# Kernel tuning notes

Hardware: AMD Instinct MI355X
Metric: run time of the kernel (lower is better)

Reference implementation:

```python
import jax, jax.numpy as jnp
import numpy as np

B = 65536
IN = 64
OUT = 256
D = 4
P = D * (D + 1) // 2  # total (w1, W2) pairs across all terms


def setup_inputs() -> dict:
    key = jax.random.key(0)
    ks = jax.random.split(key, 6)
    s = 1.0 / np.sqrt(IN)
    return {
        "x": jax.random.normal(ks[0], (B, IN), dtype=jnp.float32),
        "d0": jax.random.uniform(ks[1], (1, OUT), dtype=jnp.float32, minval=-s, maxval=s),
        "d1t_w": jax.random.uniform(ks[2], (OUT, IN), dtype=jnp.float32, minval=-s, maxval=s),
        "d1_w": jax.random.uniform(ks[3], (D, OUT, IN), dtype=jnp.float32, minval=-s, maxval=s),
        "dn_w1": jax.random.uniform(ks[4], (P, IN), dtype=jnp.float32, minval=-s, maxval=s),
        "dn_w2": jax.random.uniform(ks[5], (P, OUT, IN), dtype=jnp.float32, minval=-s, maxval=s),
    }


def reference(x, d0, d1t_w, d1_w, dn_w1, dn_w2):
    # res = d0 + d1t(x) + sum_i (x @ d1_i.T) * prod_{j<=i} (x @ (W2_ij * w1_ij).T)
    # The factorization (x @ (W2 * w1).T) is exactly equal to the original
    # Linear(in,1)(tmp_dt * (tx * W2)) chain, without the [B,out,in] intermediate.
    res = d0 + x @ d1t_w.T  # [B, OUT]
    p = 0
    for i in range(D):
        tmp = x @ d1_w[i].T  # [B, OUT]
        for _ in range(i + 1):
            M = dn_w2[p] * dn_w1[p][None, :]  # [OUT, IN]
            tmp = tmp * (x @ M.T)             # [B, OUT]
            p += 1
        res = res + tmp
    return res
```

## Files before the change

kernel.cpp:

```cpp
#include <hip/hip_runtime.h>
#include <hip/hip_bf16.h>

#define BATCH 65536
#define INF   64
#define OUTF  256
#define NMAT  15
#define RPB   256
#define LDSW  68

typedef __bf16 bf16x8 __attribute__((ext_vector_type(8)));
typedef float  f32x4  __attribute__((ext_vector_type(4)));

__device__ __forceinline__ unsigned short f2bf(float f) {
    unsigned int u = __float_as_uint(f);
    unsigned int r = (u + 0x7FFFu + ((u >> 16) & 1u)) >> 16;
    return (unsigned short)r;
}

__device__ __forceinline__ void wload(bf16x8& d, const void* p) {
    asm volatile("global_load_dwordx4 %0, %1, off" : "=v"(d) : "v"(p));
}

__global__ void build_weights(const float* __restrict__ d1t_w,
                              const float* __restrict__ d1_w,
                              const float* __restrict__ dn_w1,
                              const float* __restrict__ dn_w2,
                              unsigned short* __restrict__ wcs) {
    const int idx = blockIdx.x * 256 + threadIdx.x;
    if (idx >= NMAT * OUTF * INF / 8) return;
    const signed char kind[NMAT] = {0,1,2,1,2,2,1,2,2,2,1,2,2,2,2};
    const signed char sidx[NMAT] = {0,0,0,1,1,2,2,3,4,5,3,6,7,8,9};
    const int slot = idx >> 11, rem8 = idx & 2047;
    const int o = rem8 >> 3, cc = rem8 & 7;
    const int s = cc >> 2, g = cc & 3;
    const int i0 = cc * 8;
    const int cs = o >> 4, l = o & 15;
    const int k = kind[slot], si = sidx[slot];
    unsigned short o8[8];
#pragma unroll
    for (int j = 0; j < 8; ++j) {
        const int e = o * INF + i0 + j;
        float v;
        if (k == 0)      v = d1t_w[e];
        else if (k == 1) v = d1_w[si * OUTF * INF + e];
        else             v = dn_w2[si * OUTF * INF + e] * dn_w1[si * INF + i0 + j];
        o8[j] = f2bf(v);
    }
    char* dst = (char*)wcs + (((size_t)slot * 16 + cs) * 2 + s) * 1024 + g * 256 + l * 16;
    *(bf16x8*)dst = *(bf16x8*)o8;
}

__global__ __launch_bounds__(512, 4) void taylor_kernel(
    const float* __restrict__ x, const float* __restrict__ d0w,
    const unsigned short* __restrict__ wcs, float* __restrict__ out)
{
    __shared__ char  xsh[32768];
    __shared__ float sbuf[2][2][32 * LDSW];

    const int lane  = threadIdx.x & 63;
    const int wv    = threadIdx.x >> 6;
    const int strip = wv >> 1;
    const int role  = wv & 1;
    const int l15   = lane & 15;
    const int g     = lane >> 4;
    const int cg    = blockIdx.x >> 8;
    const int rc    = blockIdx.x & 255;
    const int cs    = cg * 4 + strip;

    const int MA[8] = {0, 1, 2, 6, 7, 8, 9, 9};
    const int MB[8] = {3, 4, 5, 10, 11, 12, 13, 14};
    bf16x8 b[8][2];
    const char* wb0 = (const char*)wcs + lane * 16;
#pragma unroll
    for (int i = 0; i < 8; ++i) {
        const int m = role ? MB[i] : MA[i];
        if (role == 0 && i == 7) continue;
        const char* wp = wb0 + (((size_t)m * 16 + cs) * 2) * 1024;
        wload(b[i][0], wp);
        wload(b[i][1], wp + 1024);
    }

    const size_t row0 = (size_t)rc * RPB;

    {
        const float* xsrc = x + row0 * INF;
#pragma unroll
        for (int j = 0; j < 4; ++j) {
            const int c = j * 512 + (int)threadIdx.x;
            f32x4 v0 = *(const f32x4*)(xsrc + (size_t)c * 8);
            f32x4 v1 = *(const f32x4*)(xsrc + (size_t)c * 8 + 4);
            bf16x8 fr;
#pragma unroll
            for (int q = 0; q < 4; ++q) { fr[q] = (__bf16)v0[q]; fr[4 + q] = (__bf16)v1[q]; }
            const int row = c >> 3, cc = c & 7;
            const int ss = cc >> 2, gg = cc & 3;
            const int grp = row >> 4, r_ = row & 15;
            const int rx = r_ ^ ((ss * 4 + gg) & 7);
            *(bf16x8*)(xsh + grp * 2048 + ss * 1024 + gg * 256 + rx * 16) = fr;
        }
    }

    asm volatile("s_waitcnt vmcnt(0)" ::: "memory");
    __builtin_amdgcn_sched_barrier(0);
    __syncthreads();

    const f32x4 d0v = *(const f32x4*)(d0w + cs * 16 + g * 4);
    const int x0off = (l15 ^ g) * 16;
    const int x1off = (l15 ^ (4 + g)) * 16;

#pragma unroll
    for (int t = 0; t < 8; ++t) {
        const char* pg0 = xsh + (t * 2) * 2048 + g * 256;
        const char* pg1 = pg0 + 2048;
        bf16x8 u00 = *(const bf16x8*)(pg0 + x0off);
        bf16x8 u01 = *(const bf16x8*)(pg0 + 1024 + x1off);
        bf16x8 u10 = *(const bf16x8*)(pg1 + x0off);
        bf16x8 u11 = *(const bf16x8*)(pg1 + 1024 + x1off);

        f32x4 res0, res1, tmp0, tmp1, y0, y1;
        const f32x4 z = {0.f, 0.f, 0.f, 0.f};
        __builtin_amdgcn_s_setprio(1);
#define Y4(bi, c0)                                                                  \
        y0 = __builtin_amdgcn_mfma_f32_16x16x32_bf16(b[bi][0], u00, c0, 0, 0, 0);   \
        y1 = __builtin_amdgcn_mfma_f32_16x16x32_bf16(b[bi][0], u10, c0, 0, 0, 0);   \
        y0 = __builtin_amdgcn_mfma_f32_16x16x32_bf16(b[bi][1], u01, y0, 0, 0, 0);   \
        y1 = __builtin_amdgcn_mfma_f32_16x16x32_bf16(b[bi][1], u11, y1, 0, 0, 0);
        if (role == 0) {
            Y4(0, d0v) res0 = y0; res1 = y1;
            Y4(1, z)   tmp0 = y0; tmp1 = y1;
            Y4(2, z)   tmp0 *= y0; tmp1 *= y1; res0 += tmp0; res1 += tmp1;
            Y4(3, z)   tmp0 = y0; tmp1 = y1;
            Y4(4, z)   tmp0 *= y0; tmp1 *= y1;
            Y4(5, z)   tmp0 *= y0; tmp1 *= y1;
            Y4(6, z)   tmp0 *= y0; tmp1 *= y1; res0 += tmp0; res1 += tmp1;
        } else {
            Y4(0, z)   tmp0 = y0; tmp1 = y1;
            Y4(1, z)   tmp0 *= y0; tmp1 *= y1;
            Y4(2, z)   tmp0 *= y0; tmp1 *= y1; res0 = tmp0; res1 = tmp1;
            Y4(3, z)   tmp0 = y0; tmp1 = y1;
            Y4(4, z)   tmp0 *= y0; tmp1 *= y1;
            Y4(5, z)   tmp0 *= y0; tmp1 *= y1;
            Y4(6, z)   tmp0 *= y0; tmp1 *= y1;
            Y4(7, z)   tmp0 *= y0; tmp1 *= y1; res0 += tmp0; res1 += tmp1;
        }
#undef Y4
        __builtin_amdgcn_s_setprio(0);

        float* sb = &sbuf[t & 1][role][0];
        const int colw = strip * 16 + g * 4;
        *(f32x4*)&sb[l15 * LDSW + colw]        = res0;
        *(f32x4*)&sb[(16 + l15) * LDSW + colw] = res1;
        asm volatile("s_waitcnt lgkmcnt(0)\n\ts_barrier" ::: "memory");

        const float* pA = &sbuf[t & 1][0][0];
        const float* pB = &sbuf[t & 1][1][0];
        const int rr = threadIdx.x >> 4;
        const int c4 = (threadIdx.x & 15) * 4;
        f32x4 v = *(const f32x4*)&pA[rr * LDSW + c4];
        v = v + *(const f32x4*)&pB[rr * LDSW + c4];
        float* op = out + (row0 + (size_t)t * 32 + rr) * OUTF + cg * 64 + c4;
        __builtin_nontemporal_store(v, (f32x4*)op);
    }
}

extern "C" void kernel_launch(void* const* d_in, const int* in_sizes, int n_in,
                              void* d_out, int out_size, void* d_ws, size_t ws_size,
                              hipStream_t stream) {
    const float* x    = (const float*)d_in[0];
    const float* d0   = (const float*)d_in[1];
    const float* d1t  = (const float*)d_in[2];
    const float* d1w  = (const float*)d_in[3];
    const float* dnw1 = (const float*)d_in[4];
    const float* dnw2 = (const float*)d_in[5];
    unsigned short* wcs = (unsigned short*)d_ws;
    float* out = (float*)d_out;

    build_weights<<<(NMAT * OUTF * INF / 8 + 255) / 256, 256, 0, stream>>>(
        d1t, d1w, dnw1, dnw2, wcs);
    taylor_kernel<<<4 * (BATCH / RPB), 512, 0, stream>>>(x, d0, wcs, out);
}
```

Measured before the change: 41.01 us.

## Split work into three balanced wave roles with narrower column groups

The block shrinks to 6 waves: 2 column strips with 3 roles each, so every wave runs exactly 5 weight matrices instead of 7 or 8 per role. The grid doubles to 8 column groups of 32 output columns, and each block reduces three partial LDS buffers before its store. MFMA chains use two independent accumulator pairs for more instruction-level parallelism, and the weight-load wait moves ahead of x staging. In exchange, each row block of x is loaded and converted to bf16 twice as often, and only 256 of 384 threads do the final store.

```diff
diff --git a/kernel.cpp b/kernel.cpp
--- a/kernel.cpp
+++ b/kernel.cpp
@@ -6,7 +6,7 @@
 #define OUTF  256
 #define NMAT  15
 #define RPB   256
-#define LDSW  68
+#define LDSW  36
 
 typedef __bf16 bf16x8 __attribute__((ext_vector_type(8)));
 typedef float  f32x4  __attribute__((ext_vector_type(4)));
@@ -50,58 +50,60 @@
     *(bf16x8*)dst = *(bf16x8*)o8;
 }
 
-__global__ __launch_bounds__(512, 4) void taylor_kernel(
+__global__ __launch_bounds__(384, 4) void taylor_kernel(
     const float* __restrict__ x, const float* __restrict__ d0w,
     const unsigned short* __restrict__ wcs, float* __restrict__ out)
 {
     __shared__ char  xsh[32768];
-    __shared__ float sbuf[2][2][32 * LDSW];
+    __shared__ float sbuf[2][3][32 * LDSW];
 
     const int lane  = threadIdx.x & 63;
     const int wv    = threadIdx.x >> 6;
-    const int strip = wv >> 1;
-    const int role  = wv & 1;
+    const int strip = (wv >= 3) ? 1 : 0;
+    const int role  = wv - 3 * strip;
     const int l15   = lane & 15;
     const int g     = lane >> 4;
     const int cg    = blockIdx.x >> 8;
     const int rc    = blockIdx.x & 255;
-    const int cs    = cg * 4 + strip;
-
-    const int MA[8] = {0, 1, 2, 6, 7, 8, 9, 9};
-    const int MB[8] = {3, 4, 5, 10, 11, 12, 13, 14};
-    bf16x8 b[8][2];
+    const int cs    = cg * 2 + strip;
+
+    const int M0a[5] = {0, 6, 7, 8, 9};
+    const int M1a[5] = {1, 2, 3, 4, 5};
+    const int M2a[5] = {10, 11, 12, 13, 14};
+    bf16x8 b[5][2];
     const char* wb0 = (const char*)wcs + lane * 16;
 #pragma unroll
-    for (int i = 0; i < 8; ++i) {
-        const int m = role ? MB[i] : MA[i];
-        if (role == 0 && i == 7) continue;
+    for (int i = 0; i < 5; ++i) {
+        const int m = (role == 0) ? M0a[i] : (role == 1) ? M1a[i] : M2a[i];
         const char* wp = wb0 + (((size_t)m * 16 + cs) * 2) * 1024;
         wload(b[i][0], wp);
         wload(b[i][1], wp + 1024);
     }
+    asm volatile("s_waitcnt vmcnt(0)" ::: "memory");
+    __builtin_amdgcn_sched_barrier(0);
 
     const size_t row0 = (size_t)rc * RPB;
 
     {
         const float* xsrc = x + row0 * INF;
 #pragma unroll
-        for (int j = 0; j < 4; ++j) {
-            const int c = j * 512 + (int)threadIdx.x;
-            f32x4 v0 = *(const f32x4*)(xsrc + (size_t)c * 8);
-            f32x4 v1 = *(const f32x4*)(xsrc + (size_t)c * 8 + 4);
-            bf16x8 fr;
-#pragma unroll
-            for (int q = 0; q < 4; ++q) { fr[q] = (__bf16)v0[q]; fr[4 + q] = (__bf16)v1[q]; }
-            const int row = c >> 3, cc = c & 7;
-            const int ss = cc >> 2, gg = cc & 3;
-            const int grp = row >> 4, r_ = row & 15;
-            const int rx = r_ ^ ((ss * 4 + gg) & 7);
-            *(bf16x8*)(xsh + grp * 2048 + ss * 1024 + gg * 256 + rx * 16) = fr;
+        for (int j = 0; j < 6; ++j) {
+            const int c = j * 384 + (int)threadIdx.x;
+            if (c < 2048) {
+                f32x4 v0 = *(const f32x4*)(xsrc + (size_t)c * 8);
+                f32x4 v1 = *(const f32x4*)(xsrc + (size_t)c * 8 + 4);
+                bf16x8 fr;
+#pragma unroll
+                for (int q = 0; q < 4; ++q) { fr[q] = (__bf16)v0[q]; fr[4 + q] = (__bf16)v1[q]; }
+                const int row = c >> 3, cc = c & 7;
+                const int ss = cc >> 2, gg = cc & 3;
+                const int grp = row >> 4, r_ = row & 15;
+                const int rx = r_ ^ ((ss * 4 + gg) & 7);
+                *(bf16x8*)(xsh + grp * 2048 + ss * 1024 + gg * 256 + rx * 16) = fr;
+            }
         }
     }
 
-    asm volatile("s_waitcnt vmcnt(0)" ::: "memory");
-    __builtin_amdgcn_sched_barrier(0);
     __syncthreads();
 
     const f32x4 d0v = *(const f32x4*)(d0w + cs * 16 + g * 4);
@@ -117,33 +119,51 @@
         bf16x8 u10 = *(const bf16x8*)(pg1 + x0off);
         bf16x8 u11 = *(const bf16x8*)(pg1 + 1024 + x1off);
 
-        f32x4 res0, res1, tmp0, tmp1, y0, y1;
+        f32x4 res0, res1, tmp0, tmp1;
+        f32x4 y0a, y0b, y1a, y1b;
         const f32x4 z = {0.f, 0.f, 0.f, 0.f};
         __builtin_amdgcn_s_setprio(1);
-#define Y4(bi, c0)                                                                  \
-        y0 = __builtin_amdgcn_mfma_f32_16x16x32_bf16(b[bi][0], u00, c0, 0, 0, 0);   \
-        y1 = __builtin_amdgcn_mfma_f32_16x16x32_bf16(b[bi][0], u10, c0, 0, 0, 0);   \
-        y0 = __builtin_amdgcn_mfma_f32_16x16x32_bf16(b[bi][1], u01, y0, 0, 0, 0);   \
-        y1 = __builtin_amdgcn_mfma_f32_16x16x32_bf16(b[bi][1], u11, y1, 0, 0, 0);
+#define YM(bi, ya, yb, c0)                                                          \
+        ya = __builtin_amdgcn_mfma_f32_16x16x32_bf16(b[bi][0], u00, c0, 0, 0, 0);   \
+        yb = __builtin_amdgcn_mfma_f32_16x16x32_bf16(b[bi][0], u10, c0, 0, 0, 0);   \
+        ya = __builtin_amdgcn_mfma_f32_16x16x32_bf16(b[bi][1], u01, ya, 0, 0, 0);   \
+        yb = __builtin_amdgcn_mfma_f32_16x16x32_bf16(b[bi][1], u11, yb, 0, 0, 0);
+
         if (role == 0) {
-            Y4(0, d0v) res0 = y0; res1 = y1;
-            Y4(1, z)   tmp0 = y0; tmp1 = y1;
-            Y4(2, z)   tmp0 *= y0; tmp1 *= y1; res0 += tmp0; res1 += tmp1;
-            Y4(3, z)   tmp0 = y0; tmp1 = y1;
-            Y4(4, z)   tmp0 *= y0; tmp1 *= y1;
-            Y4(5, z)   tmp0 *= y0; tmp1 *= y1;
-            Y4(6, z)   tmp0 *= y0; tmp1 *= y1; res0 += tmp0; res1 += tmp1;
+            YM(0, y0a, y0b, d0v)
+            YM(1, y1a, y1b, z)
+            res0 = y0a;  res1 = y0b;
+            tmp0 = y1a;  tmp1 = y1b;
+            YM(2, y0a, y0b, z)
+            YM(3, y1a, y1b, z)
+            tmp0 *= y0a; tmp1 *= y0b;
+            tmp0 *= y1a; tmp1 *= y1b;
+            YM(4, y0a, y0b, z)
+            tmp0 *= y0a; tmp1 *= y0b;
+            res0 += tmp0; res1 += tmp1;
+        } else if (role == 1) {
+            YM(0, y0a, y0b, z)
+            YM(1, y1a, y1b, z)
+            res0 = y0a * y1a; res1 = y0b * y1b;
+            YM(2, y0a, y0b, z)
+            YM(3, y1a, y1b, z)
+            tmp0 = y0a * y1a; tmp1 = y0b * y1b;
+            YM(4, y0a, y0b, z)
+            tmp0 *= y0a; tmp1 *= y0b;
+            res0 += tmp0; res1 += tmp1;
         } else {
-            Y4(0, z)   tmp0 = y0; tmp1 = y1;
-            Y4(1, z)   tmp0 *= y0; tmp1 *= y1;
-            Y4(2, z)   tmp0 *= y0; tmp1 *= y1; res0 = tmp0; res1 = tmp1;
-            Y4(3, z)   tmp0 = y0; tmp1 = y1;
-            Y4(4, z)   tmp0 *= y0; tmp1 *= y1;
-            Y4(5, z)   tmp0 *= y0; tmp1 *= y1;
-            Y4(6, z)   tmp0 *= y0; tmp1 *= y1;
-            Y4(7, z)   tmp0 *= y0; tmp1 *= y1; res0 += tmp0; res1 += tmp1;
+            YM(0, y0a, y0b, z)
+            YM(1, y1a, y1b, z)
+            tmp0 = y0a * y1a; tmp1 = y0b * y1b;
+            YM(2, y0a, y0b, z)
+            YM(3, y1a, y1b, z)
+            tmp0 *= y0a; tmp1 *= y0b;
+            tmp0 *= y1a; tmp1 *= y1b;
+            YM(4, y0a, y0b, z)
+            tmp0 *= y0a; tmp1 *= y0b;
+            res0 = tmp0; res1 = tmp1;
         }
-#undef Y4
+#undef YM
         __builtin_amdgcn_s_setprio(0);
 
         float* sb = &sbuf[t & 1][role][0];
@@ -152,14 +172,18 @@
         *(f32x4*)&sb[(16 + l15) * LDSW + colw] = res1;
         asm volatile("s_waitcnt lgkmcnt(0)\n\ts_barrier" ::: "memory");
 
-        const float* pA = &sbuf[t & 1][0][0];
-        const float* pB = &sbuf[t & 1][1][0];
-        const int rr = threadIdx.x >> 4;
-        const int c4 = (threadIdx.x & 15) * 4;
-        f32x4 v = *(const f32x4*)&pA[rr * LDSW + c4];
-        v = v + *(const f32x4*)&pB[rr * LDSW + c4];
-        float* op = out + (row0 + (size_t)t * 32 + rr) * OUTF + cg * 64 + c4;
-        __builtin_nontemporal_store(v, (f32x4*)op);
+        const int rr = threadIdx.x >> 3;
+        if (rr < 32) {
+            const int c4 = (threadIdx.x & 7) * 4;
+            const float* p0 = &sbuf[t & 1][0][0];
+            const float* p1 = &sbuf[t & 1][1][0];
+            const float* p2 = &sbuf[t & 1][2][0];
+            f32x4 v = *(const f32x4*)&p0[rr * LDSW + c4];
+            v = v + *(const f32x4*)&p1[rr * LDSW + c4];
+            v = v + *(const f32x4*)&p2[rr * LDSW + c4];
+            float* op = out + (row0 + (size_t)t * 32 + rr) * OUTF + cg * 32 + c4;
+            __builtin_nontemporal_store(v, (f32x4*)op);
+        }
     }
 }
 
@@ -177,5 +201,5 @@
 
     build_weights<<<(NMAT * OUTF * INF / 8 + 255) / 256, 256, 0, stream>>>(
         d1t, d1w, dnw1, dnw2, wcs);
-    taylor_kernel<<<4 * (BATCH / RPB), 512, 0, stream>>>(x, d0, wcs, out);
-}
+    taylor_kernel<<<8 * (BATCH / RPB), 384, 0, stream>>>(x, d0, wcs, out);
+}
```

Measured after the change: 63.29 us. 1.54x slower.
